# Kernel optimization log

Measured on AMD Instinct MI355X. Metric: run time of the kernel, lower is better.

Reference implementation:

```python
import jax, jax.numpy as jnp
import numpy as np

B, T, H = 2, 2048, 1024
NH = 16
D = H // NH  # head_dim = 64
SCALE = D ** -0.5


def setup_inputs() -> dict:
    key = jax.random.key(0)
    ks = jax.random.split(key, 10)
    s_in = 1.0 / np.sqrt(H)   # torch Linear init scale for fan_in=H
    s_d = 1.0 / np.sqrt(D)
    return {
        "x":  jax.random.normal(ks[0], (B, T, H), jnp.float32),
        # stacked per-head Q/K projections: [NH, H, D] weights, [NH, D] biases
        "Wq": jax.random.uniform(ks[1], (NH, H, D), jnp.float32, -s_in, s_in),
        "bq": jax.random.uniform(ks[2], (NH, D), jnp.float32, -s_in, s_in),
        "Wk": jax.random.uniform(ks[3], (NH, H, D), jnp.float32, -s_in, s_in),
        "bk": jax.random.uniform(ks[4], (NH, D), jnp.float32, -s_in, s_in),
        # shared V projection H->D
        "Wv": jax.random.uniform(ks[5], (H, D), jnp.float32, -s_in, s_in),
        "bv": jax.random.uniform(ks[6], (D,), jnp.float32, -s_in, s_in),
        # out projection D->H
        "Wo": jax.random.uniform(ks[7], (D, H), jnp.float32, -s_d, s_d),
        "bo": jax.random.uniform(ks[8], (H,), jnp.float32, -s_d, s_d),
    }


def reference(x, Wq, bq, Wk, bk, Wv, bv, Wo, bo):
    # shared value projection: [B,T,D]
    v = jnp.einsum('bth,hd->btd', x, Wv) + bv
    # batched per-head Q/K projections: [NH,B,T,D]
    q = jnp.einsum('bth,nhd->nbtd', x, Wq) + bq[:, None, None, :]
    k = jnp.einsum('bth,nhd->nbtd', x, Wk) + bk[:, None, None, :]
    # scaled causal attention scores: [NH,B,T,T]
    scores = jnp.einsum('nbtd,nbsd->nbts', q, k) * SCALE
    causal = jnp.triu(jnp.ones((T, T), bool), k=1)  # True above diagonal
    scores = jnp.where(causal, -jnp.inf, scores)
    weights = jax.nn.softmax(scores, axis=-1)  # dropout is identity in eval
    # shared V attended per head, then mean over heads: [B,T,D]
    mean_head = jnp.einsum('nbts,bsd->btd', weights, v) / NH
    out = jnp.einsum('btd,dh->bth', mean_head, Wo) + bo
    mean_weights = jnp.mean(weights, axis=0)  # [B,T,T]
    return out, mean_weights
```

## Files before the change

### kernel.cpp

```cpp
#include <hip/hip_runtime.h>
#include <hip/hip_bf16.h>

#define B_ 2
#define T_ 2048
#define H_ 1024
#define NH_ 16
#define D_ 64
#define BT_ (B_*T_)
#define SCALE_ 0.125f
#define LOG2E_ 1.4426950408889634f

typedef _Float16 f16x8 __attribute__((ext_vector_type(8)));
typedef float f32x4 __attribute__((ext_vector_type(4)));

#define MFMA(a,b,c) __builtin_amdgcn_mfma_f32_16x16x32_f16((a),(b),(c),0,0,0)
#define EXP2(x) __builtin_amdgcn_exp2f(x)

typedef const __attribute__((address_space(1))) void GV;
typedef __attribute__((address_space(3))) void LV;

__device__ __forceinline__ size_t toff(int r, int c, int C) {
    return (size_t)((r >> 4) * (C >> 5) + (c >> 5)) * 512 + (size_t)(((c & 31) >> 3) * 128 + (r & 15) * 8 + (c & 7));
}
__device__ __forceinline__ f16x8 frag_ld(const _Float16* base, int rt, int kc, int Cc, int l15, int quad) {
    return *(const f16x8*)(base + (size_t)(rt * Cc + kc) * 512 + quad * 128 + l15 * 8);
}

__global__ __launch_bounds__(256) void k_prep(const float* __restrict__ x,
                                              const float* __restrict__ Wq, const float* __restrict__ Wk,
                                              const float* __restrict__ Wv, const float* __restrict__ Wo,
                                              _Float16* __restrict__ xb, _Float16* __restrict__ wqk,
                                              _Float16* __restrict__ wvt, _Float16* __restrict__ wot,
                                              float* __restrict__ mw) {
    int blk = blockIdx.x, tid = threadIdx.x;
    if (blk < 2048) {
        int idx = blk * 256 + tid;
        int t = idx >> 7, h0 = (idx & 127) * 8;
        const float* p = x + ((size_t)t << 10) + h0;
        float4 f0 = *(const float4*)p;
        float4 f1 = *(const float4*)(p + 4);
        f16x8 o;
        o[0]=(_Float16)f0.x; o[1]=(_Float16)f0.y; o[2]=(_Float16)f0.z; o[3]=(_Float16)f0.w;
        o[4]=(_Float16)f1.x; o[5]=(_Float16)f1.y; o[6]=(_Float16)f1.z; o[7]=(_Float16)f1.w;
        *(f16x8*)(xb + toff(t, h0, 1024)) = o;
    } else if (blk < 2560) {
        int idx = (blk - 2048) * 256 + tid;
        int head = idx >> 13;
        int rem = idx & 8191;
        int h = rem >> 3;
        int d0 = (rem & 7) * 8;
        const float* pq = Wq + ((size_t)((head << 10) + h)) * 64 + d0;
        const float* pk = Wk + ((size_t)((head << 10) + h)) * 64 + d0;
        float4 q0 = *(const float4*)pq, q1 = *(const float4*)(pq + 4);
        float4 k0 = *(const float4*)pk, k1 = *(const float4*)(pk + 4);
        float qv[8] = {q0.x,q0.y,q0.z,q0.w,q1.x,q1.y,q1.z,q1.w};
        float kv[8] = {k0.x,k0.y,k0.z,k0.w,k1.x,k1.y,k1.z,k1.w};
#pragma unroll
        for (int e = 0; e < 8; e++) {
            int c = head * 64 + d0 + e;
            wqk[toff(c, h, 1024)]        = (_Float16)qv[e];
            wqk[toff(c + 1024, h, 1024)] = (_Float16)kv[e];
        }
    } else if (blk < 2816) {
        int i = (blk - 2560) * 256 + tid;
        int d = i >> 10, h = i & 1023;
        wvt[toff(d, h, 1024)] = (_Float16)Wv[(size_t)h * 64 + d];
        int hh = i >> 6, dd = i & 63;
        wot[toff(hh, dd, 64)] = (_Float16)Wo[(size_t)dd * 1024 + hh];
    } else {
        int iz = blk - 2816;
        int b = (iz >= 496) ? 1 : 0;
        int i = iz - b * 496;
        int s64 = (int)((sqrtf(8.f * i + 1.f) + 1.f) * 0.5f);
        if (s64 * (s64 - 1) / 2 > i) s64--;
        if ((s64 + 1) * s64 / 2 <= i) s64++;
        int q64 = i - s64 * (s64 - 1) / 2;
        float4 z = {0.f, 0.f, 0.f, 0.f};
#pragma unroll
        for (int it = 0; it < 4; it++) {
            int idx = it * 256 + tid;
            int r = idx >> 4, c4 = idx & 15;
            *(float4*)&mw[(size_t)(b * T_ + q64 * 64 + r) * T_ + s64 * 64 + c4 * 4] = z;
        }
    }
}

__global__ __launch_bounds__(256) void k_gemm(const _Float16* __restrict__ xb, const _Float16* __restrict__ wqk,
                                              const float* __restrict__ bq, const float* __restrict__ bk,
                                              const _Float16* __restrict__ wvt, const float* __restrict__ bv,
                                              _Float16* __restrict__ qh, _Float16* __restrict__ kh,
                                              _Float16* __restrict__ vt) {
    __shared__ __align__(16) unsigned char smem[32768];
    _Float16* As = (_Float16*)smem;
    _Float16* Bs = (_Float16*)(smem + 16384);
    int tid = threadIdx.x, w = tid >> 6, lane = tid & 63, l15 = lane & 15, quad = lane >> 4;
    if (blockIdx.x >= 512) {
        float (*red)[16][64] = (float(*)[16][64])smem;
        int rt = blockIdx.x - 512;
        f32x4 acc[4];
#pragma unroll
        for (int j = 0; j < 4; j++) acc[j] = (f32x4){0.f, 0.f, 0.f, 0.f};
        for (int q = 0; q < 8; q++) {
            int kc = w * 8 + q;
            f16x8 a = frag_ld(xb, rt, kc, 32, l15, quad);
#pragma unroll
            for (int j = 0; j < 4; j++) {
                f16x8 bb = frag_ld(wvt, j, kc, 32, l15, quad);
                acc[j] = MFMA(a, bb, acc[j]);
            }
        }
#pragma unroll
        for (int j = 0; j < 4; j++)
#pragma unroll
            for (int r = 0; r < 4; r++) red[w][quad * 4 + r][j * 16 + l15] = acc[j][r];
        __syncthreads();
        int r = tid >> 4, dg = tid & 15;
        int b = rt >> 7, tt = (rt & 127) * 16 + r;
        _Float16* vtb = vt + (size_t)b * 131072;
#pragma unroll
        for (int e = 0; e < 4; e++) {
            int d = dg * 4 + e;
            float s = red[0][r][d] + red[1][r][d] + red[2][r][d] + red[3][r][d] + bv[d];
            vtb[toff(d, tt, 2048)] = (_Float16)s;
        }
        return;
    }
    int bm = blockIdx.x >> 4, bn = blockIdx.x & 15;
    int rowbase = (w >> 1) * 64, colbase = (w & 1) * 64;
    f32x4 acc[4][4];
#pragma unroll
    for (int i = 0; i < 4; i++)
#pragma unroll
        for (int j = 0; j < 4; j++) acc[i][j] = (f32x4){0.f, 0.f, 0.f, 0.f};

    for (int kk = 0; kk < 16; kk++) {
        __syncthreads();
#pragma unroll
        for (int p = 0; p < 4; p++) {
            int c = w * 4 + p;
            __builtin_amdgcn_global_load_lds((GV*)(xb  + ((size_t)((bm * 8 + (c >> 1)) * 32 + kk * 2 + (c & 1))) * 512 + lane * 8),
                                             (LV*)(As + c * 512 + lane * 8), 16, 0, 0);
            __builtin_amdgcn_global_load_lds((GV*)(wqk + ((size_t)((bn * 8 + (c >> 1)) * 32 + kk * 2 + (c & 1))) * 512 + lane * 8),
                                             (LV*)(Bs + c * 512 + lane * 8), 16, 0, 0);
        }
        __syncthreads();
#pragma unroll
        for (int kc = 0; kc < 2; kc++) {
            f16x8 a[4], bf[4];
#pragma unroll
            for (int i = 0; i < 4; i++) a[i]  = *(const f16x8*)&As[((rowbase >> 4) + i) * 1024 + kc * 512 + quad * 128 + l15 * 8];
#pragma unroll
            for (int j = 0; j < 4; j++) bf[j] = *(const f16x8*)&Bs[((colbase >> 4) + j) * 1024 + kc * 512 + quad * 128 + l15 * 8];
#pragma unroll
            for (int i = 0; i < 4; i++)
#pragma unroll
                for (int j = 0; j < 4; j++) acc[i][j] = MFMA(a[i], bf[j], acc[i][j]);
        }
    }
    __syncthreads();
    int b = (bm * 128) >> 11;
    int t_base = (bm * 128) & 2047;
    int rtbase = (t_base + rowbase) >> 4;
    bool isq = (bn < 8);
    int c2base = isq ? (bn * 128 + colbase) : (bn * 128 + colbase - 1024);
    int n = c2base >> 6;
    _Float16* dst = (isq ? qh : kh) + (size_t)(n * 2 + b) * 131072;
    const float* bias_p = isq ? bq : bk;
    float qs = SCALE_ * LOG2E_;
    int i2 = lane >> 4, rowrb = lane & 15;
#pragma unroll
    for (int j = 0; j < 4; j++) {
        float bias = bias_p[c2base + j * 16 + l15];
        _Float16* stg = ((j & 1) ? Bs : As) + w * 1024;
#pragma unroll
        for (int i = 0; i < 4; i++)
#pragma unroll
            for (int r = 0; r < 4; r++) {
                float v = acc[i][j][r] + bias;
                if (isq) v *= qs;
                stg[(i * 16 + quad * 4 + r) * 16 + l15] = (_Float16)v;
            }
#pragma unroll
        for (int oct = 0; oct < 2; oct++) {
            f16x8 val = *(const f16x8*)&stg[(i2 * 16 + rowrb) * 16 + oct * 8];
            int dd0 = j * 16 + oct * 8;
            *(f16x8*)(dst + (size_t)((rtbase + i2) * 2 + (dd0 >> 5)) * 512 + ((dd0 & 31) >> 3) * 128 + rowrb * 8) = val;
        }
    }
}

__global__ __launch_bounds__(256) void k_pass1(const _Float16* __restrict__ qh, const _Float16* __restrict__ kh,
                                               float* __restrict__ lstat4) {
    int tid = threadIdx.x, w = tid >> 6, lane = tid & 63, l15 = lane & 15, quad = lane >> 4;
    int blk = blockIdx.x;
    int n = blk >> 6, b = (blk >> 5) & 1, strip = blk & 31;
    const _Float16* qb = qh + (size_t)(n * 2 + b) * 131072;
    const _Float16* kp = kh + (size_t)(n * 2 + b) * 131072;
    int rt0 = strip * 4;
    f16x8 aq[4][2];
#pragma unroll
    for (int i = 0; i < 4; i++)
#pragma unroll
        for (int kk = 0; kk < 2; kk++) aq[i][kk] = frag_ld(qb, rt0 + i, kk, 2, l15, quad);
    float l[4][4];
#pragma unroll
    for (int i = 0; i < 4; i++)
#pragma unroll
        for (int r = 0; r < 4; r++) l[i][r] = 0.f;
    int st_lo = w * (strip + 1);
    int st_hi = st_lo + strip + 1;
    for (int st = st_lo; st < st_hi; st++) {
        f16x8 c0 = frag_ld(kp, st, 0, 2, l15, quad);
        f16x8 c1 = frag_ld(kp, st, 1, 2, l15, quad);
#pragma unroll
        for (int i = 0; i < 4; i++) {
            if (st > rt0 + i) continue;
            f32x4 sc = (f32x4){0.f, 0.f, 0.f, 0.f};
            sc = MFMA(aq[i][0], c0, sc);
            sc = MFMA(aq[i][1], c1, sc);
            if (st == rt0 + i) {
#pragma unroll
                for (int r = 0; r < 4; r++)
                    if (l15 <= quad * 4 + r) l[i][r] += EXP2(sc[r]);
            } else {
#pragma unroll
                for (int r = 0; r < 4; r++) l[i][r] += EXP2(sc[r]);
            }
        }
    }
#pragma unroll
    for (int off = 1; off < 16; off <<= 1)
#pragma unroll
        for (int i = 0; i < 4; i++)
#pragma unroll
            for (int r = 0; r < 4; r++) l[i][r] += __shfl_xor(l[i][r], off, 64);
    if (l15 == 0) {
        int base = (n * 2 + b) * 2048 + strip * 64;
#pragma unroll
        for (int i = 0; i < 4; i++)
#pragma unroll
            for (int r = 0; r < 4; r++)
                lstat4[(size_t)(base + i * 16 + quad * 4 + r) * 4 + w] = l[i][r];
    }
}

__global__ __launch_bounds__(256, 4) void k_pass2(const _Float16* __restrict__ qh, const _Float16* __restrict__ kh,
                                                  const float* __restrict__ lstat4,
                                                  float* __restrict__ mw, _Float16* __restrict__ mwh) {
    __shared__ float sl[16][128];
    __shared__ __align__(16) _Float16 kst[2][4096];
    int blk = blockIdx.x;
    int b = (blk >= 272) ? 1 : 0;
    int i0 = blk - 272 * b;
    int i = (i0 & 7) * 34 + (i0 >> 3);
    int p = (int)((sqrtf(4.f * i + 1.f) - 1.f) * 0.5f);
    while (p * (p + 1) > i) p--;
    while ((p + 1) * (p + 2) <= i) p++;
    int s64 = i - p * (p + 1);
    bool masked = (s64 >= 2 * p);
    int tid = threadIdx.x, w = tid >> 6, lane = tid & 63, l15 = lane & 15, quad = lane >> 4;
    for (int ii = tid; ii < 2048; ii += 256) {
        int h = ii >> 7, r = ii & 127;
        const float4 pl = *(const float4*)&lstat4[(size_t)((h * 2 + b) * 2048 + p * 128 + r) * 4];
        sl[h][r] = 0.0625f / (pl.x + pl.y + pl.z + pl.w);
    }
    int rw = w * 32;
    int rt0 = p * 8 + w * 2;
    int st0 = s64 * 4;
    f32x4 macc[2][4];
#pragma unroll
    for (int ii = 0; ii < 2; ii++)
#pragma unroll
        for (int j = 0; j < 4; j++) macc[ii][j] = (f32x4){0.f, 0.f, 0.f, 0.f};

    {
        const _Float16* kp = kh + (size_t)b * 131072;
#pragma unroll
        for (int inst = 0; inst < 2; inst++) {
            int c = inst * 4 + w;
            int gc = (st0 + (c >> 1)) * 2 + (c & 1);
            __builtin_amdgcn_global_load_lds((GV*)(kp + (size_t)gc * 512 + lane * 8),
                                             (LV*)(kst[0] + c * 512 + lane * 8), 16, 0, 0);
        }
    }
    __syncthreads();

    for (int n = 0; n < NH_; n++) {
        if (n < NH_ - 1) {
            const _Float16* kp = kh + (size_t)((n + 1) * 2 + b) * 131072;
#pragma unroll
            for (int inst = 0; inst < 2; inst++) {
                int c = inst * 4 + w;
                int gc = (st0 + (c >> 1)) * 2 + (c & 1);
                __builtin_amdgcn_global_load_lds((GV*)(kp + (size_t)gc * 512 + lane * 8),
                                                 (LV*)(kst[(n + 1) & 1] + c * 512 + lane * 8), 16, 0, 0);
            }
        }
        const _Float16* qb = qh + (size_t)(n * 2 + b) * 131072;
        f16x8 A[2][2];
#pragma unroll
        for (int ii = 0; ii < 2; ii++)
#pragma unroll
            for (int kc = 0; kc < 2; kc++) A[ii][kc] = frag_ld(qb, rt0 + ii, kc, 2, l15, quad);
        f32x4 slv[2];
#pragma unroll
        for (int ii = 0; ii < 2; ii++) slv[ii] = *(const f32x4*)&sl[n][rw + ii * 16 + quad * 4];
        const _Float16* ks = kst[n & 1];
#pragma unroll
        for (int j = 0; j < 4; j++) {
            f16x8 K0 = *(const f16x8*)&ks[(j * 2 + 0) * 512 + quad * 128 + l15 * 8];
            f16x8 K1 = *(const f16x8*)&ks[(j * 2 + 1) * 512 + quad * 128 + l15 * 8];
#pragma unroll
            for (int ii = 0; ii < 2; ii++) {
                f32x4 sc = (f32x4){0.f, 0.f, 0.f, 0.f};
                sc = MFMA(A[ii][0], K0, sc);
                sc = MFMA(A[ii][1], K1, sc);
                if (masked) {
                    int sg = s64 * 64 + j * 16 + l15;
#pragma unroll
                    for (int r = 0; r < 4; r++) {
                        int tg = p * 128 + rw + ii * 16 + quad * 4 + r;
                        macc[ii][j][r] += (sg <= tg) ? EXP2(sc[r]) * slv[ii][r] : 0.f;
                    }
                } else {
#pragma unroll
                    for (int r = 0; r < 4; r++) macc[ii][j][r] += EXP2(sc[r]) * slv[ii][r];
                }
            }
        }
        __syncthreads();
    }
    float* mwb = mw + (size_t)b * T_ * T_;
#pragma unroll
    for (int ii = 0; ii < 2; ii++)
#pragma unroll
        for (int j = 0; j < 4; j++)
#pragma unroll
            for (int r = 0; r < 4; r++) {
                int tg = p * 128 + rw + ii * 16 + quad * 4 + r;
                int sg = s64 * 64 + j * 16 + l15;
                mwb[(size_t)tg * T_ + sg] = macc[ii][j][r];
            }
    _Float16* mhb = mwh + (size_t)b * 4194304;
    _Float16* ws16 = kst[0] + w * 1024;
    int rowrb = lane & 15, qc = lane >> 4;
#pragma unroll
    for (int cc = 0; cc < 2; cc++) {
#pragma unroll
        for (int ii = 0; ii < 2; ii++)
#pragma unroll
            for (int j2 = 0; j2 < 2; j2++)
#pragma unroll
                for (int r = 0; r < 4; r++) {
                    int clw = j2 * 16 + l15;
                    ws16[ii * 512 + (clw >> 3) * 128 + (quad * 4 + r) * 8 + (clw & 7)] =
                        (_Float16)macc[ii][cc * 2 + j2][r];
                }
#pragma unroll
        for (int ii = 0; ii < 2; ii++) {
            f16x8 val = *(const f16x8*)&ws16[ii * 512 + qc * 128 + rowrb * 8];
            *(f16x8*)(mhb + (size_t)((rt0 + ii) * 64 + (s64 * 2 + cc)) * 512 + qc * 128 + rowrb * 8) = val;
        }
    }
}

__global__ __launch_bounds__(256) void k_pass3a(const _Float16* __restrict__ mwh, const _Float16* __restrict__ vt,
                                                _Float16* __restrict__ mhp) {
    __shared__ float red[4][16][64];
    int tid = threadIdx.x, w = tid >> 6, lane = tid & 63, l15 = lane & 15, quad = lane >> 4;
    int blk = blockIdx.x;
    int tile = blk >> 2, q = blk & 3;
    int b = tile >> 7, rtb = tile & 127;
    const _Float16* mb = mwh + (size_t)b * 4194304;
    const _Float16* vb = vt + (size_t)b * 131072;
    int nkc = (rtb * 16 + 47) >> 5;
    int qlo = q * 16;
    int qhi = min(qlo + 16, nkc);
    f32x4 acc[4];
#pragma unroll
    for (int j = 0; j < 4; j++) acc[j] = (f32x4){0.f, 0.f, 0.f, 0.f};
    for (int kc = qlo + w; kc < qhi; kc += 4) {
        f16x8 a = frag_ld(mb, rtb, kc, 64, l15, quad);
#pragma unroll
        for (int j = 0; j < 4; j++) {
            f16x8 bb = frag_ld(vb, j, kc, 64, l15, quad);
            acc[j] = MFMA(a, bb, acc[j]);
        }
    }
#pragma unroll
    for (int j = 0; j < 4; j++)
#pragma unroll
        for (int r = 0; r < 4; r++) red[w][quad * 4 + r][j * 16 + l15] = acc[j][r];
    __syncthreads();
    int r = tid >> 4, dg = tid & 15;
    _Float16* dst = mhp + (size_t)q * 262144;
#pragma unroll
    for (int e = 0; e < 4; e++) {
        int d = dg * 4 + e;
        float s = red[0][r][d] + red[1][r][d] + red[2][r][d] + red[3][r][d];
        dst[toff(tile * 16 + r, d, 64)] = (_Float16)s;
    }
}

__global__ __launch_bounds__(256) void k_pass3b(const _Float16* __restrict__ mhp, const _Float16* __restrict__ wot,
                                                const float* __restrict__ bo, float* __restrict__ out0) {
    int bm = blockIdx.x >> 4, bn = blockIdx.x & 15;
    int tid = threadIdx.x, w = tid >> 6, lane = tid & 63, l15 = lane & 15, quad = lane >> 4;
    int rt = bm * 4 + w;
    f16x8 a0[4], a1[4];
#pragma unroll
    for (int q = 0; q < 4; q++) {
        const _Float16* mb = mhp + (size_t)q * 262144;
        a0[q] = frag_ld(mb, rt, 0, 2, l15, quad);
        a1[q] = frag_ld(mb, rt, 1, 2, l15, quad);
    }
    f32x4 acc[4];
#pragma unroll
    for (int j = 0; j < 4; j++) acc[j] = (f32x4){0.f, 0.f, 0.f, 0.f};
#pragma unroll
    for (int j = 0; j < 4; j++) {
        f16x8 b0 = frag_ld(wot, bn * 4 + j, 0, 2, l15, quad);
        f16x8 b1 = frag_ld(wot, bn * 4 + j, 1, 2, l15, quad);
#pragma unroll
        for (int q = 0; q < 4; q++) {
            acc[j] = MFMA(a0[q], b0, acc[j]);
            acc[j] = MFMA(a1[q], b1, acc[j]);
        }
    }
#pragma unroll
    for (int j = 0; j < 4; j++)
#pragma unroll
        for (int r = 0; r < 4; r++) {
            int row = rt * 16 + quad * 4 + r;
            int col = bn * 64 + j * 16 + l15;
            out0[(size_t)row * 1024 + col] = acc[j][r] + bo[col];
        }
}

extern "C" void kernel_launch(void* const* d_in, const int* in_sizes, int n_in,
                              void* d_out, int out_size, void* d_ws, size_t ws_size,
                              hipStream_t stream) {
    const float* x  = (const float*)d_in[0];
    const float* Wq = (const float*)d_in[1];
    const float* bq = (const float*)d_in[2];
    const float* Wk = (const float*)d_in[3];
    const float* bk = (const float*)d_in[4];
    const float* Wv = (const float*)d_in[5];
    const float* bv = (const float*)d_in[6];
    const float* Wo = (const float*)d_in[7];
    const float* bo = (const float*)d_in[8];
    char* ws = (char*)d_ws;
    _Float16* xb    = (_Float16*)(ws + 0);
    _Float16* wqk   = (_Float16*)(ws + 8388608);
    _Float16* wvt   = (_Float16*)(ws + 12582912);
    _Float16* mwh   = (_Float16*)(ws + 0);
    _Float16* qh    = (_Float16*)(ws + 16777216);
    _Float16* kh    = (_Float16*)(ws + 25165824);
    _Float16* vt    = (_Float16*)(ws + 33554432);
    float*    lstat4= (float*)   (ws + 34078720);
    _Float16* mhp   = (_Float16*)(ws + 35127296);
    _Float16* wot   = (_Float16*)(ws + 37224448);
    float* out0 = (float*)d_out;
    float* mw   = out0 + (size_t)BT_ * H_;

    k_prep   <<<3808, 256, 0, stream>>>(x, Wq, Wk, Wv, Wo, xb, wqk, wvt, wot, mw);
    k_gemm   <<<768,  256, 0, stream>>>(xb, wqk, bq, bk, wvt, bv, qh, kh, vt);
    k_pass1  <<<1024, 256, 0, stream>>>(qh, kh, lstat4);
    k_pass2  <<<544,  256, 0, stream>>>(qh, kh, lstat4, mw, mwh);
    k_pass3a <<<1024, 256, 0, stream>>>(mwh, vt, mhp);
    k_pass3b <<<1024, 256, 0, stream>>>(mhp, wot, bo, out0);
}
```

Baseline: 206.1 us.

## Halve attention pass tiles, balance pass1 key split, fold normalizer into MFMA accumulator

Pass1 now handles 32-row strips instead of 64, doubling its grid, and spreads the key tiles evenly across the four waves. Pass2 now uses 64x64 tiles instead of 128x64, roughly doubling its block count. This reduces wasted work on the causal diagonal and improves load balance across CUs. The per-row normalizer is turned into a log2 offset that seeds the MFMA accumulator, replacing a multiply per element. The cost is that each Q tile is loaded by more blocks, and that K tiles and per-block setup are reused across less work.

```diff
diff --git a/kernel.cpp b/kernel.cpp
--- a/kernel.cpp
+++ b/kernel.cpp
@@ -193,27 +193,28 @@
                                                float* __restrict__ lstat4) {
     int tid = threadIdx.x, w = tid >> 6, lane = tid & 63, l15 = lane & 15, quad = lane >> 4;
     int blk = blockIdx.x;
-    int n = blk >> 6, b = (blk >> 5) & 1, strip = blk & 31;
+    int n = blk >> 7, b = (blk >> 6) & 1, s2 = blk & 63;
     const _Float16* qb = qh + (size_t)(n * 2 + b) * 131072;
     const _Float16* kp = kh + (size_t)(n * 2 + b) * 131072;
-    int rt0 = strip * 4;
-    f16x8 aq[4][2];
-#pragma unroll
-    for (int i = 0; i < 4; i++)
+    int rt0 = s2 * 2;
+    f16x8 aq[2][2];
+#pragma unroll
+    for (int i = 0; i < 2; i++)
 #pragma unroll
         for (int kk = 0; kk < 2; kk++) aq[i][kk] = frag_ld(qb, rt0 + i, kk, 2, l15, quad);
-    float l[4][4];
-#pragma unroll
-    for (int i = 0; i < 4; i++)
+    float l[2][4];
+#pragma unroll
+    for (int i = 0; i < 2; i++)
 #pragma unroll
         for (int r = 0; r < 4; r++) l[i][r] = 0.f;
-    int st_lo = w * (strip + 1);
-    int st_hi = st_lo + strip + 1;
+    int total = 2 * s2 + 2;
+    int st_lo = (w * total) >> 2;
+    int st_hi = ((w + 1) * total) >> 2;
     for (int st = st_lo; st < st_hi; st++) {
         f16x8 c0 = frag_ld(kp, st, 0, 2, l15, quad);
         f16x8 c1 = frag_ld(kp, st, 1, 2, l15, quad);
 #pragma unroll
-        for (int i = 0; i < 4; i++) {
+        for (int i = 0; i < 2; i++) {
             if (st > rt0 + i) continue;
             f32x4 sc = (f32x4){0.f, 0.f, 0.f, 0.f};
             sc = MFMA(aq[i][0], c0, sc);
@@ -231,13 +232,13 @@
 #pragma unroll
     for (int off = 1; off < 16; off <<= 1)
 #pragma unroll
-        for (int i = 0; i < 4; i++)
+        for (int i = 0; i < 2; i++)
 #pragma unroll
             for (int r = 0; r < 4; r++) l[i][r] += __shfl_xor(l[i][r], off, 64);
     if (l15 == 0) {
-        int base = (n * 2 + b) * 2048 + strip * 64;
-#pragma unroll
-        for (int i = 0; i < 4; i++)
+        int base = (n * 2 + b) * 2048 + s2 * 32;
+#pragma unroll
+        for (int i = 0; i < 2; i++)
 #pragma unroll
             for (int r = 0; r < 4; r++)
                 lstat4[(size_t)(base + i * 16 + quad * 4 + r) * 4 + w] = l[i][r];
@@ -247,31 +248,29 @@
 __global__ __launch_bounds__(256, 4) void k_pass2(const _Float16* __restrict__ qh, const _Float16* __restrict__ kh,
                                                   const float* __restrict__ lstat4,
                                                   float* __restrict__ mw, _Float16* __restrict__ mwh) {
-    __shared__ float sl[16][128];
+    __shared__ float sl[16][64];
     __shared__ __align__(16) _Float16 kst[2][4096];
     int blk = blockIdx.x;
-    int b = (blk >= 272) ? 1 : 0;
-    int i0 = blk - 272 * b;
-    int i = (i0 & 7) * 34 + (i0 >> 3);
-    int p = (int)((sqrtf(4.f * i + 1.f) - 1.f) * 0.5f);
-    while (p * (p + 1) > i) p--;
-    while ((p + 1) * (p + 2) <= i) p++;
-    int s64 = i - p * (p + 1);
-    bool masked = (s64 >= 2 * p);
+    int b = (blk >= 528) ? 1 : 0;
+    int i0 = blk - 528 * b;
+    int i = (i0 & 7) * 66 + (i0 >> 3);
+    int p = (int)((sqrtf(8.f * i + 1.f) - 1.f) * 0.5f);
+    while (p * (p + 1) / 2 > i) p--;
+    while ((p + 1) * (p + 2) / 2 <= i) p++;
+    int s64 = i - p * (p + 1) / 2;
+    bool masked = (s64 == p);
     int tid = threadIdx.x, w = tid >> 6, lane = tid & 63, l15 = lane & 15, quad = lane >> 4;
-    for (int ii = tid; ii < 2048; ii += 256) {
-        int h = ii >> 7, r = ii & 127;
-        const float4 pl = *(const float4*)&lstat4[(size_t)((h * 2 + b) * 2048 + p * 128 + r) * 4];
-        sl[h][r] = 0.0625f / (pl.x + pl.y + pl.z + pl.w);
-    }
-    int rw = w * 32;
-    int rt0 = p * 8 + w * 2;
+    for (int ii = tid; ii < 1024; ii += 256) {
+        int h = ii >> 6, r = ii & 63;
+        const float4 pl = *(const float4*)&lstat4[(size_t)((h * 2 + b) * 2048 + p * 64 + r) * 4];
+        sl[h][r] = -(__log2f(pl.x + pl.y + pl.z + pl.w) + 4.0f);
+    }
+    int rw = w * 16;
+    int rt0 = p * 4 + w;
     int st0 = s64 * 4;
-    f32x4 macc[2][4];
-#pragma unroll
-    for (int ii = 0; ii < 2; ii++)
-#pragma unroll
-        for (int j = 0; j < 4; j++) macc[ii][j] = (f32x4){0.f, 0.f, 0.f, 0.f};
+    f32x4 macc[4];
+#pragma unroll
+    for (int j = 0; j < 4; j++) macc[j] = (f32x4){0.f, 0.f, 0.f, 0.f};
 
     {
         const _Float16* kp = kh + (size_t)b * 131072;
@@ -297,70 +296,54 @@
             }
         }
         const _Float16* qb = qh + (size_t)(n * 2 + b) * 131072;
-        f16x8 A[2][2];
-#pragma unroll
-        for (int ii = 0; ii < 2; ii++)
-#pragma unroll
-            for (int kc = 0; kc < 2; kc++) A[ii][kc] = frag_ld(qb, rt0 + ii, kc, 2, l15, quad);
-        f32x4 slv[2];
-#pragma unroll
-        for (int ii = 0; ii < 2; ii++) slv[ii] = *(const f32x4*)&sl[n][rw + ii * 16 + quad * 4];
+        f16x8 A0 = frag_ld(qb, rt0, 0, 2, l15, quad);
+        f16x8 A1 = frag_ld(qb, rt0, 1, 2, l15, quad);
+        f32x4 slv = *(const f32x4*)&sl[n][rw + quad * 4];
         const _Float16* ks = kst[n & 1];
 #pragma unroll
         for (int j = 0; j < 4; j++) {
             f16x8 K0 = *(const f16x8*)&ks[(j * 2 + 0) * 512 + quad * 128 + l15 * 8];
             f16x8 K1 = *(const f16x8*)&ks[(j * 2 + 1) * 512 + quad * 128 + l15 * 8];
-#pragma unroll
-            for (int ii = 0; ii < 2; ii++) {
-                f32x4 sc = (f32x4){0.f, 0.f, 0.f, 0.f};
-                sc = MFMA(A[ii][0], K0, sc);
-                sc = MFMA(A[ii][1], K1, sc);
-                if (masked) {
-                    int sg = s64 * 64 + j * 16 + l15;
-#pragma unroll
-                    for (int r = 0; r < 4; r++) {
-                        int tg = p * 128 + rw + ii * 16 + quad * 4 + r;
-                        macc[ii][j][r] += (sg <= tg) ? EXP2(sc[r]) * slv[ii][r] : 0.f;
-                    }
-                } else {
-#pragma unroll
-                    for (int r = 0; r < 4; r++) macc[ii][j][r] += EXP2(sc[r]) * slv[ii][r];
+            f32x4 sc = slv;
+            sc = MFMA(A0, K0, sc);
+            sc = MFMA(A1, K1, sc);
+            if (masked) {
+                int sg = s64 * 64 + j * 16 + l15;
+#pragma unroll
+                for (int r = 0; r < 4; r++) {
+                    int tg = p * 64 + rw + quad * 4 + r;
+                    macc[j][r] += (sg <= tg) ? EXP2(sc[r]) : 0.f;
                 }
+            } else {
+#pragma unroll
+                for (int r = 0; r < 4; r++) macc[j][r] += EXP2(sc[r]);
             }
         }
         __syncthreads();
     }
     float* mwb = mw + (size_t)b * T_ * T_;
 #pragma unroll
-    for (int ii = 0; ii < 2; ii++)
-#pragma unroll
-        for (int j = 0; j < 4; j++)
-#pragma unroll
-            for (int r = 0; r < 4; r++) {
-                int tg = p * 128 + rw + ii * 16 + quad * 4 + r;
-                int sg = s64 * 64 + j * 16 + l15;
-                mwb[(size_t)tg * T_ + sg] = macc[ii][j][r];
-            }
+    for (int j = 0; j < 4; j++)
+#pragma unroll
+        for (int r = 0; r < 4; r++) {
+            int tg = p * 64 + rw + quad * 4 + r;
+            int sg = s64 * 64 + j * 16 + l15;
+            mwb[(size_t)tg * T_ + sg] = macc[j][r];
+        }
     _Float16* mhb = mwh + (size_t)b * 4194304;
     _Float16* ws16 = kst[0] + w * 1024;
     int rowrb = lane & 15, qc = lane >> 4;
 #pragma unroll
     for (int cc = 0; cc < 2; cc++) {
 #pragma unroll
-        for (int ii = 0; ii < 2; ii++)
-#pragma unroll
-            for (int j2 = 0; j2 < 2; j2++)
-#pragma unroll
-                for (int r = 0; r < 4; r++) {
-                    int clw = j2 * 16 + l15;
-                    ws16[ii * 512 + (clw >> 3) * 128 + (quad * 4 + r) * 8 + (clw & 7)] =
-                        (_Float16)macc[ii][cc * 2 + j2][r];
-                }
-#pragma unroll
-        for (int ii = 0; ii < 2; ii++) {
-            f16x8 val = *(const f16x8*)&ws16[ii * 512 + qc * 128 + rowrb * 8];
-            *(f16x8*)(mhb + (size_t)((rt0 + ii) * 64 + (s64 * 2 + cc)) * 512 + qc * 128 + rowrb * 8) = val;
-        }
+        for (int j2 = 0; j2 < 2; j2++)
+#pragma unroll
+            for (int r = 0; r < 4; r++) {
+                int clw = j2 * 16 + l15;
+                ws16[(clw >> 3) * 128 + (quad * 4 + r) * 8 + (clw & 7)] = (_Float16)macc[cc * 2 + j2][r];
+            }
+        f16x8 val = *(const f16x8*)&ws16[qc * 128 + rowrb * 8];
+        *(f16x8*)(mhb + (size_t)(rt0 * 64 + (s64 * 2 + cc)) * 512 + qc * 128 + rowrb * 8) = val;
     }
 }
 
@@ -465,8 +448,8 @@
 
     k_prep   <<<3808, 256, 0, stream>>>(x, Wq, Wk, Wv, Wo, xb, wqk, wvt, wot, mw);
     k_gemm   <<<768,  256, 0, stream>>>(xb, wqk, bq, bk, wvt, bv, qh, kh, vt);
-    k_pass1  <<<1024, 256, 0, stream>>>(qh, kh, lstat4);
-    k_pass2  <<<544,  256, 0, stream>>>(qh, kh, lstat4, mw, mwh);
+    k_pass1  <<<2048, 256, 0, stream>>>(qh, kh, lstat4);
+    k_pass2  <<<1056, 256, 0, stream>>>(qh, kh, lstat4, mw, mwh);
     k_pass3a <<<1024, 256, 0, stream>>>(mwh, vt, mhp);
     k_pass3b <<<1024, 256, 0, stream>>>(mhp, wot, bo, out0);
 }
```

After: 196.9 us. 4.5% less time.
